# Optimization experiments

Measured on AMD Instinct MI355X. Metric: run time of the kernel, lower is better.

Reference implementation:

```python
import jax, jax.numpy as jnp
import numpy as np
import math

B, S, DIM = 2, 2048, 2048
H, NOPE, ROPE, VDIM = 16, 128, 64, 128
Q_RANK, KV_RANK = 1024, 512
EPS = 1e-6
ROPE_THETA = 10000.0


def setup_inputs() -> dict:
    key = jax.random.key(0)
    ks = jax.random.split(key, 9)
    s = 0.02  # init scale to keep activations/logits well-conditioned
    return {
        "x": jax.random.normal(ks[0], (B, S, DIM), jnp.float32),
        "wq_down": jax.random.normal(ks[1], (Q_RANK, DIM), jnp.float32) * s,
        "q_norm_w": jnp.ones((Q_RANK,), jnp.float32),
        "wq_up": jax.random.normal(ks[2], (H * NOPE, Q_RANK), jnp.float32) * s,
        "wq_rope": jax.random.normal(ks[3], (H * ROPE, Q_RANK), jnp.float32) * s,
        "wkv_down": jax.random.normal(ks[4], (KV_RANK, DIM), jnp.float32) * s,
        "kv_norm_w": jnp.ones((KV_RANK,), jnp.float32),
        "wkv_up": jax.random.normal(ks[5], (H * (NOPE + VDIM), KV_RANK), jnp.float32) * s,
        "wk_rope": jax.random.normal(ks[6], (ROPE, DIM), jnp.float32) * s,
        "wo": jax.random.normal(ks[7], (DIM, H * VDIM), jnp.float32) * s,
    }


def _rmsnorm(x, w, eps=EPS):
    return x * jax.lax.rsqrt(jnp.mean(x * x, axis=-1, keepdims=True) + eps) * w


def _rope_cos_sin(seq_len, head_dim, dtype=jnp.float32):
    inv_freq = 1.0 / (ROPE_THETA ** (jnp.arange(0, head_dim, 2, dtype=jnp.float32) / head_dim))
    t = jnp.arange(seq_len, dtype=jnp.float32)
    freqs = jnp.outer(t, inv_freq)  # [S, head_dim/2]
    return jnp.cos(freqs).astype(dtype), jnp.sin(freqs).astype(dtype)


def _apply_rope(x, cos, sin):
    # x: [B, S, h, d]; cos/sin: [S, d/2]; interleaved (complex) rotation
    x1, x2 = x[..., 0::2], x[..., 1::2]
    c = cos[None, :, None, :]
    s = sin[None, :, None, :]
    o1 = x1 * c - x2 * s
    o2 = x1 * s + x2 * c
    return jnp.stack([o1, o2], axis=-1).reshape(x.shape)


def reference(x, wq_down, q_norm_w, wq_up, wq_rope, wkv_down, kv_norm_w, wkv_up, wk_rope, wo):
    bs, seq_len, _ = x.shape
    # low-rank Q path
    q_c = _rmsnorm(x @ wq_down.T, q_norm_w)                       # [B,S,Qr]
    q_nope = (q_c @ wq_up.T).reshape(bs, seq_len, H, NOPE)
    q_pe = (q_c @ wq_rope.T).reshape(bs, seq_len, H, ROPE)
    # low-rank KV path
    kv_c = _rmsnorm(x @ wkv_down.T, kv_norm_w)                    # [B,S,KVr]
    kv_up = (x_kv := kv_c @ wkv_up.T).reshape(bs, seq_len, H, NOPE + VDIM)
    k_nope, v = kv_up[..., :NOPE], kv_up[..., NOPE:]
    k_rope_shared = (x @ wk_rope.T).reshape(bs, seq_len, 1, ROPE)
    # decoupled RoPE
    cos, sin = _rope_cos_sin(seq_len, ROPE, x.dtype)
    q_pe = _apply_rope(q_pe, cos, sin)
    k_rope_shared = _apply_rope(k_rope_shared, cos, sin)
    k_rope = jnp.broadcast_to(k_rope_shared, (bs, seq_len, H, ROPE))
    q = jnp.concatenate([q_nope, q_pe], axis=-1)                  # [B,S,H,NOPE+ROPE]
    k = jnp.concatenate([k_nope, k_rope], axis=-1)
    scale = 1.0 / math.sqrt(NOPE + ROPE)
    scores = jnp.einsum("bqhd,bkhd->bhqk", q, k) * scale          # [B,H,S,S]
    causal = jnp.tril(jnp.ones((seq_len, seq_len), bool))
    scores = jnp.where(causal[None, None], scores, -jnp.inf)
    probs = jax.nn.softmax(scores.astype(jnp.float32), axis=-1).astype(q.dtype)
    out = jnp.einsum("bhqk,bkhv->bqhv", probs, v).reshape(bs, seq_len, H * VDIM)
    return out @ wo.T
```

## Files before the change

kernel.cpp:

```cpp
#include <hip/hip_runtime.h>
#include <hip/hip_bf16.h>
#include <math.h>

#define B_    2
#define S_    2048
#define DIM_  2048
#define H_    16
#define NOPE_ 128
#define ROPE_ 64
#define VDIM_ 128
#define QR_   1024
#define KVR_  512
#define TOK_  (B_ * S_)

typedef __attribute__((ext_vector_type(8))) short short8;
typedef __attribute__((ext_vector_type(4))) float f32x4;

__device__ __forceinline__ unsigned short f2bf(float f) {
  union { float f; unsigned u; } v; v.f = f;
  unsigned r = v.u + 0x7fffu + ((v.u >> 16) & 1u);
  return (unsigned short)(r >> 16);
}
__device__ __forceinline__ unsigned pk2(float lo, float hi) {
  return (unsigned)f2bf(lo) | ((unsigned)f2bf(hi) << 16);
}

__device__ __forceinline__ void gl_lds16(const unsigned short* g, unsigned short* lds_base) {
  __builtin_amdgcn_global_load_lds(
      (const __attribute__((address_space(1))) void*)g,
      (__attribute__((address_space(3))) void*)lds_base,
      16, 0, 0);
}

__device__ __forceinline__ void store_out(float* p, float v) { *p = v; }
__device__ __forceinline__ void store_out(unsigned short* p, float v) { *p = f2bf(v); }

#define C_X    (TOK_ * DIM_ / 8)
#define C_WQD  (QR_ * DIM_ / 8)
#define C_WKVD (KVR_ * DIM_ / 8)
#define C_WKR  (ROPE_ * DIM_ / 8)
#define C_WQU  (H_ * NOPE_ * QR_ / 8)
#define C_WQR  (H_ * ROPE_ * QR_ / 8)
#define C_WKVU (H_ * (NOPE_ + VDIM_) * KVR_ / 8)
#define C_WO   (DIM_ * H_ * VDIM_ / 8)
#define C_TOT  (C_X + C_WQD + C_WKVD + C_WKR + C_WQU + C_WQR + C_WKVU + C_WO)

__global__ __launch_bounds__(256) void cvt_all(
    const float* __restrict__ x, const float* __restrict__ wqd, const float* __restrict__ wkvd,
    const float* __restrict__ wkr, const float* __restrict__ wqu, const float* __restrict__ wqr,
    const float* __restrict__ wkvu, const float* __restrict__ wo,
    unsigned short* __restrict__ xo, unsigned short* __restrict__ wqdo,
    unsigned short* __restrict__ wkvdo, unsigned short* __restrict__ wkro,
    unsigned short* __restrict__ wquo, unsigned short* __restrict__ wqro,
    unsigned short* __restrict__ wkvuo, unsigned short* __restrict__ woo) {
  int i = blockIdx.x * 256 + threadIdx.x;
  if (i >= C_TOT) return;
  const float* in; unsigned short* out;
  if (i < C_X) { in = x; out = xo; }
  else if ((i -= C_X) < C_WQD) { in = wqd; out = wqdo; }
  else if ((i -= C_WQD) < C_WKVD) { in = wkvd; out = wkvdo; }
  else if ((i -= C_WKVD) < C_WKR) { in = wkr; out = wkro; }
  else if ((i -= C_WKR) < C_WQU) { in = wqu; out = wquo; }
  else if ((i -= C_WQU) < C_WQR) { in = wqr; out = wqro; }
  else if ((i -= C_WQR) < C_WKVU) { in = wkvu; out = wkvuo; }
  else { i -= C_WKVU; in = wo; out = woo; }
  float4 f0 = *(const float4*)(in + (size_t)i * 8);
  float4 f1 = *(const float4*)(in + (size_t)i * 8 + 4);
  uint4 u;
  u.x = pk2(f0.x, f0.y); u.y = pk2(f0.z, f0.w);
  u.z = pk2(f1.x, f1.y); u.w = pk2(f1.z, f1.w);
  *(uint4*)&out[(size_t)i * 8] = u;
}

template <typename OutT, int NT>
__global__ __launch_bounds__(256) void gemm_bf16(const unsigned short* __restrict__ A,
                                                 const unsigned short* __restrict__ Bm,
                                                 OutT* __restrict__ C,
                                                 int M, int N, int K) {
  constexpr int BN = NT * 32;
  __shared__ unsigned short As[128 * 32];
  __shared__ unsigned short Bs[BN * 32];
  const int tid  = threadIdx.x;
  const int wave = tid >> 6;
  const int lane = tid & 63;
  const int quad = lane >> 4;
  const int l15  = lane & 15;
  const int m0 = blockIdx.y * 128;
  const int n0 = blockIdx.x * BN;
  const int wm = (wave & 1) * 64;
  const int wn = (wave >> 1) * (NT * 16);

  f32x4 acc[4][NT];
#pragma unroll
  for (int i = 0; i < 4; ++i)
#pragma unroll
    for (int j = 0; j < NT; ++j) {
      f32x4 z = {0.f, 0.f, 0.f, 0.f};
      acc[i][j] = z;
    }

  for (int k0 = 0; k0 < K; k0 += 32) {
    __syncthreads();
#pragma unroll
    for (int i = 0; i < 2; ++i) {
      const int s = i * 256 + tid;
      const int srow = s >> 2;
      const int sq = (s & 3) ^ ((srow >> 1) & 3);
      gl_lds16(A + (size_t)(m0 + srow) * K + k0 + sq * 8, &As[(i * 256 + wave * 64) * 8]);
    }
#pragma unroll
    for (int i = 0; i < BN / 64; ++i) {
      const int s = i * 256 + tid;
      const int srow = s >> 2;
      const int sq = (s & 3) ^ ((srow >> 1) & 3);
      const int rb = min(n0 + srow, N - 1);
      gl_lds16(Bm + (size_t)rb * K + k0 + sq * 8, &Bs[(i * 256 + wave * 64) * 8]);
    }
    __syncthreads();

    short8 a[4], b[NT];
#pragma unroll
    for (int i = 0; i < 4; ++i) {
      const int r = wm + i * 16 + l15;
      a[i] = *(const short8*)&As[(r * 4 + (quad ^ ((r >> 1) & 3))) * 8];
    }
#pragma unroll
    for (int j = 0; j < NT; ++j) {
      const int r = wn + j * 16 + l15;
      b[j] = *(const short8*)&Bs[(r * 4 + (quad ^ ((r >> 1) & 3))) * 8];
    }
#pragma unroll
    for (int i = 0; i < 4; ++i)
#pragma unroll
      for (int j = 0; j < NT; ++j)
        acc[i][j] = __builtin_amdgcn_mfma_f32_16x16x32_bf16(a[i], b[j], acc[i][j], 0, 0, 0);
  }

#pragma unroll
  for (int i = 0; i < 4; ++i) {
#pragma unroll
    for (int j = 0; j < NT; ++j) {
      const int col = n0 + wn + j * 16 + l15;
      if (col < N) {
#pragma unroll
        for (int r = 0; r < 4; ++r) {
          const int row = m0 + wm + i * 16 + quad * 4 + r;
          store_out(&C[(size_t)row * N + col], acc[i][j][r]);
        }
      }
    }
  }
}

__global__ __launch_bounds__(256) void gemm_down(const unsigned short* __restrict__ A,
                                                 const unsigned short* __restrict__ Bq,
                                                 const unsigned short* __restrict__ Bkv,
                                                 const unsigned short* __restrict__ Bkr,
                                                 float* __restrict__ Cq,
                                                 float* __restrict__ Ckv,
                                                 float* __restrict__ Ckr) {
  constexpr int K = DIM_;
  __shared__ unsigned short As[128 * 32];
  __shared__ unsigned short Bs[128 * 32];
  const int tid  = threadIdx.x;
  const int wave = tid >> 6;
  const int lane = tid & 63;
  const int quad = lane >> 4;
  const int l15  = lane & 15;
  const int m0 = blockIdx.y * 128;
  const int t  = blockIdx.x;

  const unsigned short* Bm; float* C; int n0, NB;
  if (t < 8)       { Bm = Bq;  C = Cq;  n0 = t * 128;        NB = QR_;  }
  else if (t < 12) { Bm = Bkv; C = Ckv; n0 = (t - 8) * 128;  NB = KVR_; }
  else             { Bm = Bkr; C = Ckr; n0 = 0;              NB = ROPE_; }

  const int wm = (wave & 1) * 64;
  const int wn = (wave >> 1) * 64;

  f32x4 acc[4][4];
#pragma unroll
  for (int i = 0; i < 4; ++i)
#pragma unroll
    for (int j = 0; j < 4; ++j) { f32x4 z = {0.f, 0.f, 0.f, 0.f}; acc[i][j] = z; }

  for (int k0 = 0; k0 < K; k0 += 32) {
    __syncthreads();
#pragma unroll
    for (int i = 0; i < 2; ++i) {
      const int s = i * 256 + tid;
      const int srow = s >> 2;
      const int sq = (s & 3) ^ ((srow >> 1) & 3);
      gl_lds16(A + (size_t)(m0 + srow) * K + k0 + sq * 8, &As[(i * 256 + wave * 64) * 8]);
    }
#pragma unroll
    for (int i = 0; i < 2; ++i) {
      const int s = i * 256 + tid;
      const int srow = s >> 2;
      const int sq = (s & 3) ^ ((srow >> 1) & 3);
      const int rb = min(n0 + srow, NB - 1);
      gl_lds16(Bm + (size_t)rb * K + k0 + sq * 8, &Bs[(i * 256 + wave * 64) * 8]);
    }
    __syncthreads();

    short8 a[4], b[4];
#pragma unroll
    for (int i = 0; i < 4; ++i) {
      const int r = wm + i * 16 + l15;
      a[i] = *(const short8*)&As[(r * 4 + (quad ^ ((r >> 1) & 3))) * 8];
    }
#pragma unroll
    for (int j = 0; j < 4; ++j) {
      const int r = wn + j * 16 + l15;
      b[j] = *(const short8*)&Bs[(r * 4 + (quad ^ ((r >> 1) & 3))) * 8];
    }
#pragma unroll
    for (int i = 0; i < 4; ++i)
#pragma unroll
      for (int j = 0; j < 4; ++j)
        acc[i][j] = __builtin_amdgcn_mfma_f32_16x16x32_bf16(a[i], b[j], acc[i][j], 0, 0, 0);
  }

#pragma unroll
  for (int i = 0; i < 4; ++i) {
#pragma unroll
    for (int j = 0; j < 4; ++j) {
      const int col = n0 + wn + j * 16 + l15;
      if (col < NB) {
#pragma unroll
        for (int r = 0; r < 4; ++r) {
          const int row = m0 + wm + i * 16 + quad * 4 + r;
          C[(size_t)row * NB + col] = acc[i][j][r];
        }
      }
    }
  }
}

__global__ __launch_bounds__(256) void gemm_upq(const unsigned short* __restrict__ A,
                                                const unsigned short* __restrict__ Bn,
                                                const unsigned short* __restrict__ Br,
                                                unsigned short* __restrict__ Cn,
                                                float* __restrict__ Cr) {
  constexpr int K = QR_;
  __shared__ unsigned short As[128 * 32];
  __shared__ unsigned short Bs[128 * 32];
  const int tid  = threadIdx.x;
  const int wave = tid >> 6;
  const int lane = tid & 63;
  const int quad = lane >> 4;
  const int l15  = lane & 15;
  const int m0 = blockIdx.y * 128;
  const int t  = blockIdx.x;
  const bool isn = (t < 16);
  const unsigned short* Bm = isn ? Bn : Br;
  const int n0 = isn ? t * 128 : (t - 16) * 128;
  const int NB = isn ? (H_ * NOPE_) : (H_ * ROPE_);

  const int wm = (wave & 1) * 64;
  const int wn = (wave >> 1) * 64;

  f32x4 acc[4][4];
#pragma unroll
  for (int i = 0; i < 4; ++i)
#pragma unroll
    for (int j = 0; j < 4; ++j) { f32x4 z = {0.f, 0.f, 0.f, 0.f}; acc[i][j] = z; }

  for (int k0 = 0; k0 < K; k0 += 32) {
    __syncthreads();
#pragma unroll
    for (int i = 0; i < 2; ++i) {
      const int s = i * 256 + tid;
      const int srow = s >> 2;
      const int sq = (s & 3) ^ ((srow >> 1) & 3);
      gl_lds16(A + (size_t)(m0 + srow) * K + k0 + sq * 8, &As[(i * 256 + wave * 64) * 8]);
    }
#pragma unroll
    for (int i = 0; i < 2; ++i) {
      const int s = i * 256 + tid;
      const int srow = s >> 2;
      const int sq = (s & 3) ^ ((srow >> 1) & 3);
      const int rb = min(n0 + srow, NB - 1);
      gl_lds16(Bm + (size_t)rb * K + k0 + sq * 8, &Bs[(i * 256 + wave * 64) * 8]);
    }
    __syncthreads();

    short8 a[4], b[4];
#pragma unroll
    for (int i = 0; i < 4; ++i) {
      const int r = wm + i * 16 + l15;
      a[i] = *(const short8*)&As[(r * 4 + (quad ^ ((r >> 1) & 3))) * 8];
    }
#pragma unroll
    for (int j = 0; j < 4; ++j) {
      const int r = wn + j * 16 + l15;
      b[j] = *(const short8*)&Bs[(r * 4 + (quad ^ ((r >> 1) & 3))) * 8];
    }
#pragma unroll
    for (int i = 0; i < 4; ++i)
#pragma unroll
      for (int j = 0; j < 4; ++j)
        acc[i][j] = __builtin_amdgcn_mfma_f32_16x16x32_bf16(a[i], b[j], acc[i][j], 0, 0, 0);
  }

#pragma unroll
  for (int i = 0; i < 4; ++i) {
#pragma unroll
    for (int j = 0; j < 4; ++j) {
      const int col = n0 + wn + j * 16 + l15;
#pragma unroll
      for (int r = 0; r < 4; ++r) {
        const int row = m0 + wm + i * 16 + quad * 4 + r;
        if (isn) Cn[(size_t)row * (H_ * NOPE_) + col] = f2bf(acc[i][j][r]);
        else     Cr[(size_t)row * (H_ * ROPE_) + col] = acc[i][j][r];
      }
    }
  }
}

__global__ __launch_bounds__(256) void rmsnorm2(const float* __restrict__ xq,
                                                const float* __restrict__ wq,
                                                unsigned short* __restrict__ oq,
                                                const float* __restrict__ xkv,
                                                const float* __restrict__ wkv,
                                                unsigned short* __restrict__ okv) {
  __shared__ float red[256];
  const bool isq = (blockIdx.y == 0);
  const int n = isq ? QR_ : KVR_;
  const float* x = isq ? xq : xkv;
  const float* w = isq ? wq : wkv;
  unsigned short* o = isq ? oq : okv;
  const int row = blockIdx.x;
  const float* p = x + (size_t)row * n;
  float s = 0.f;
  for (int i = threadIdx.x; i < n; i += 256) { float v = p[i]; s += v * v; }
  red[threadIdx.x] = s;
  __syncthreads();
  for (int off = 128; off > 0; off >>= 1) {
    if (threadIdx.x < off) red[threadIdx.x] += red[threadIdx.x + off];
    __syncthreads();
  }
  const float inv = rsqrtf(red[0] / (float)n + 1e-6f);
  unsigned short* po = o + (size_t)row * n;
  for (int i = threadIdx.x; i < n; i += 256) po[i] = f2bf(p[i] * inv * w[i]);
}

#define PAIRS_Q (TOK_ * H_ * 32)
#define PAIRS_K (TOK_ * 32)

__global__ void rope_all(const float* __restrict__ qin, unsigned short* __restrict__ qout,
                         const float* __restrict__ kin, unsigned short* __restrict__ kout) {
  int idx = blockIdx.x * blockDim.x + threadIdx.x;
  if (idx >= PAIRS_Q + PAIRS_K) return;
  int heads, id;
  const float* xin; unsigned short* xout;
  if (idx < PAIRS_Q) { heads = H_; xin = qin; xout = qout; id = idx; }
  else { heads = 1; xin = kin; xout = kout; id = idx - PAIRS_Q; }
  const int i = id & 31;
  const int h = (id >> 5) % heads;
  const int row = id / (32 * heads);
  const int pos = row & (S_ - 1);
  const float freq = expf(-9.210340371976184f * (float)i / 32.0f);
  const float ang = (float)pos * freq;
  const float c = cosf(ang), sn = sinf(ang);
  const float* p = xin + ((size_t)row * heads + h) * 64 + 2 * i;
  unsigned short* q = xout + ((size_t)row * heads + h) * 64 + 2 * i;
  const float x1 = p[0], x2 = p[1];
  q[0] = f2bf(x1 * c - x2 * sn);
  q[1] = f2bf(x1 * sn + x2 * c);
}

__global__ __launch_bounds__(256) void transpose_v(const unsigned short* __restrict__ kv_up,
                                                   unsigned short* __restrict__ vt_g) {
  __shared__ unsigned short T[128 * 72];
  const int tid = threadIdx.x;
  const int k0 = blockIdx.x * 64;
  const int h = blockIdx.y, b = blockIdx.z;
  const size_t tok0 = (size_t)b * S_;
#pragma unroll
  for (int i = 0; i < 2; ++i) {
    const int u = i * 256 + tid;
    const int kp = u >> 4, c8 = u & 15;
    const unsigned short* p0 =
        kv_up + (tok0 + k0 + 2 * kp) * (size_t)(H_ * 256) + h * 256 + NOPE_ + c8 * 8;
    union { uint4 v; unsigned short s[8]; } r0, r1;
    r0.v = *(const uint4*)p0;
    r1.v = *(const uint4*)(p0 + H_ * 256);
#pragma unroll
    for (int j = 0; j < 8; ++j)
      *(unsigned*)&T[(c8 * 8 + j) * 72 + 2 * kp] = (unsigned)r0.s[j] | ((unsigned)r1.s[j] << 16);
  }
  __syncthreads();
#pragma unroll
  for (int i = 0; i < 4; ++i) {
    const int sl = i * 256 + tid;
    const int f = sl >> 3, c = sl & 7;
    *(uint4*)(vt_g + ((size_t)(b * H_ + h) * 128 + f) * S_ + k0 + c * 8) =
        *(const uint4*)&T[f * 72 + c * 8];
  }
}

#define LV 72

__global__ __launch_bounds__(512) void flash_attn_mfma(const unsigned short* q_nope,
                                                       const unsigned short* __restrict__ q_pe,
                                                       const unsigned short* __restrict__ kv_up,
                                                       const unsigned short* __restrict__ k_rope,
                                                       const unsigned short* __restrict__ vt_g,
                                                       unsigned short* attn_o) {
  __shared__ unsigned short Ksn[2][64 * 16 * 8];
  __shared__ unsigned short Ksr[2][64 * 8 * 8];
  __shared__ unsigned short Vt[128 * 8 * 8];
  __shared__ unsigned short Ps[128 * LV];

  const int tid  = threadIdx.x;
  const int wave = tid >> 6;
  const int lane = tid & 63;
  const int quad = lane >> 4;
  const int l15  = lane & 15;
  const int pair = blockIdx.x;
  const int h  = blockIdx.y;
  const int b  = blockIdx.z;
  const size_t tok0 = (size_t)b * S_;
  const float scale2 = 0.07216878364870323f * 1.4426950408889634f;
  const int qtA = 15 - pair;
  const int qtB = pair;
  const int n0  = 2 * qtA + 2;

  auto LOADQ = [&](short8* qf, int qt) {
    const size_t qrow = tok0 + qt * 128 + wave * 16 + l15;
    const unsigned short* pn = q_nope + qrow * (size_t)(H_ * NOPE_) + h * NOPE_;
    const unsigned short* pp = q_pe + qrow * (size_t)(H_ * ROPE_) + h * ROPE_;
#pragma unroll
    for (int s = 0; s < 4; ++s) qf[s] = *(const short8*)(pn + s * 32 + quad * 8);
#pragma unroll
    for (int s = 4; s < 6; ++s) qf[s] = *(const short8*)(pp + (s - 4) * 32 + quad * 8);
  };

  auto STAGE_K = [&](int bi, int kt) {
    const int k0 = kt * 64;
#pragma unroll
    for (int i = 0; i < 2; ++i) {
      const int sl = i * 512 + tid;
      const int key = sl >> 4;
      const int c = (sl & 15) ^ (key & 15);
      gl_lds16(kv_up + (tok0 + k0 + key) * (size_t)(H_ * 256) + h * 256 + c * 8,
               &Ksn[bi][(i * 512 + wave * 64) * 8]);
    }
    {
      const int sl = tid;
      const int key = sl >> 3;
      const int c = (sl & 7) ^ (key & 7);
      gl_lds16(k_rope + (tok0 + k0 + key) * (size_t)ROPE_ + c * 8,
               &Ksr[bi][(wave * 64) * 8]);
    }
  };
  auto STAGE_V = [&](int kt) {
    const int k0 = kt * 64;
#pragma unroll
    for (int i = 0; i < 2; ++i) {
      const int sl = i * 512 + tid;
      const int f = sl >> 3;
      const int c = (sl & 7) ^ (f & 7);
      gl_lds16(vt_g + ((size_t)(b * H_ + h) * 128 + f) * S_ + k0 + c * 8,
               &Vt[(i * 512 + wave * 64) * 8]);
    }
  };

  short8 qf[6];
  LOADQ(qf, qtA);

  float m_st[4], l_st[4];
  f32x4 o[8];
#pragma unroll
  for (int r = 0; r < 4; ++r) { m_st[r] = -1e30f; l_st[r] = 0.f; }
#pragma unroll
  for (int nt = 0; nt < 8; ++nt) { f32x4 z = {0.f, 0.f, 0.f, 0.f}; o[nt] = z; }

  auto EPI = [&](int qt) {
    float invl[4];
#pragma unroll
    for (int r = 0; r < 4; ++r) invl[r] = 1.f / l_st[r];
#pragma unroll
    for (int nt = 0; nt < 8; ++nt)
#pragma unroll
      for (int r = 0; r < 4; ++r) {
        const size_t row = tok0 + qt * 128 + wave * 16 + quad * 4 + r;
        attn_o[row * (size_t)(H_ * VDIM_) + h * VDIM_ + nt * 16 + l15] =
            f2bf(o[nt][r] * invl[r]);
      }
  };

  STAGE_K(0, 0);

  for (int it = 0; it < 34; ++it) {
    const int cur = it & 1;
    const int nxt = cur ^ 1;
    const bool ph1 = (it >= n0);
    const int qt = ph1 ? qtB : qtA;
    const int kt = ph1 ? (it - n0) : it;
    const bool last = (it + 1 >= 34);
    const bool active = !(kt == 2 * qt + 1 && wave < 4);

    __builtin_amdgcn_s_barrier();
    asm volatile("" ::: "memory");

    STAGE_V(kt);
    if (!last) {
      const bool p1n = (it + 1 >= n0);
      const int kt2 = p1n ? (it + 1 - n0) : (it + 1);
      STAGE_K(nxt, kt2);
      asm volatile("s_waitcnt vmcnt(5)" ::: "memory");
    } else {
      asm volatile("s_waitcnt vmcnt(2)" ::: "memory");
    }
    __builtin_amdgcn_s_barrier();
    asm volatile("" ::: "memory");
    __builtin_amdgcn_sched_barrier(0);

    if (active) {
      f32x4 sacc[4];
#pragma unroll
      for (int nt = 0; nt < 4; ++nt) { f32x4 z = {0.f, 0.f, 0.f, 0.f}; sacc[nt] = z; }
      __builtin_amdgcn_s_setprio(1);
#pragma unroll
      for (int s = 0; s < 4; ++s) {
#pragma unroll
        for (int nt = 0; nt < 4; ++nt) {
          const int key = nt * 16 + l15;
          short8 kb = *(const short8*)&Ksn[cur][(key * 16 + ((s * 4 + quad) ^ (key & 15))) * 8];
          sacc[nt] = __builtin_amdgcn_mfma_f32_16x16x32_bf16(qf[s], kb, sacc[nt], 0, 0, 0);
        }
      }
#pragma unroll
      for (int s = 4; s < 6; ++s) {
#pragma unroll
        for (int nt = 0; nt < 4; ++nt) {
          const int key = nt * 16 + l15;
          short8 kb = *(const short8*)&Ksr[cur][(key * 8 + (((s - 4) * 4 + quad) ^ (key & 7))) * 8];
          sacc[nt] = __builtin_amdgcn_mfma_f32_16x16x32_bf16(qf[s], kb, sacc[nt], 0, 0, 0);
        }
      }
      __builtin_amdgcn_s_setprio(0);

      float sc[4][4];
#pragma unroll
      for (int nt = 0; nt < 4; ++nt)
#pragma unroll
        for (int r = 0; r < 4; ++r) sc[nt][r] = sacc[nt][r] * scale2;
      if (kt >= 2 * qt) {
        const int koff = (kt - 2 * qt) * 64;
        const int rw = wave * 16 + quad * 4;
#pragma unroll
        for (int nt = 0; nt < 4; ++nt)
#pragma unroll
          for (int r = 0; r < 4; ++r)
            if ((koff + nt * 16 + l15) > (rw + r)) sc[nt][r] = -1e30f;
      }

      float mt[4];
#pragma unroll
      for (int r = 0; r < 4; ++r)
        mt[r] = fmaxf(fmaxf(sc[0][r], sc[1][r]), fmaxf(sc[2][r], sc[3][r]));
#pragma unroll
      for (int mask = 1; mask <= 8; mask <<= 1)
#pragma unroll
        for (int r = 0; r < 4; ++r) mt[r] = fmaxf(mt[r], __shfl_xor(mt[r], mask, 64));

      float al[4], rs[4];
#pragma unroll
      for (int r = 0; r < 4; ++r) {
        const float mn = fmaxf(m_st[r], mt[r]);
        al[r] = exp2f(m_st[r] - mn);
        m_st[r] = mn;
        rs[r] = 0.f;
      }
#pragma unroll
      for (int nt = 0; nt < 4; ++nt)
#pragma unroll
        for (int r = 0; r < 4; ++r) {
          const float p = exp2f(sc[nt][r] - m_st[r]);
          sc[nt][r] = p;
          rs[r] += p;
        }
#pragma unroll
      for (int mask = 1; mask <= 8; mask <<= 1)
#pragma unroll
        for (int r = 0; r < 4; ++r) rs[r] += __shfl_xor(rs[r], mask, 64);
#pragma unroll
      for (int r = 0; r < 4; ++r) l_st[r] = l_st[r] * al[r] + rs[r];

#pragma unroll
      for (int nt = 0; nt < 4; ++nt)
#pragma unroll
        for (int r = 0; r < 4; ++r)
          Ps[(wave * 16 + quad * 4 + r) * LV + nt * 16 + l15] = f2bf(sc[nt][r]);
      __builtin_amdgcn_wave_barrier();

#pragma unroll
      for (int nt = 0; nt < 8; ++nt)
#pragma unroll
        for (int r = 0; r < 4; ++r) o[nt][r] *= al[r];
    }

    if (!last) {
      asm volatile("s_waitcnt vmcnt(3)" ::: "memory");
    } else {
      asm volatile("s_waitcnt vmcnt(0)" ::: "memory");
    }
    __builtin_amdgcn_s_barrier();
    asm volatile("" ::: "memory");
    __builtin_amdgcn_sched_barrier(0);

    if (active) {
      __builtin_amdgcn_s_setprio(1);
#pragma unroll
      for (int s = 0; s < 2; ++s) {
        short8 pa = *(const short8*)&Ps[(wave * 16 + l15) * LV + s * 32 + quad * 8];
#pragma unroll
        for (int nt = 0; nt < 8; ++nt) {
          const int f = nt * 16 + l15;
          short8 vb = *(const short8*)&Vt[(f * 8 + ((s * 4 + quad) ^ (f & 7))) * 8];
          o[nt] = __builtin_amdgcn_mfma_f32_16x16x32_bf16(pa, vb, o[nt], 0, 0, 0);
        }
      }
      __builtin_amdgcn_s_setprio(0);
    }

    if (it == n0 - 1) {
      EPI(qtA);
      LOADQ(qf, qtB);
#pragma unroll
      for (int r = 0; r < 4; ++r) { m_st[r] = -1e30f; l_st[r] = 0.f; }
#pragma unroll
      for (int nt = 0; nt < 8; ++nt) { f32x4 z = {0.f, 0.f, 0.f, 0.f}; o[nt] = z; }
    }
  }

  EPI(qtB);
}

extern "C" void kernel_launch(void* const* d_in, const int* in_sizes, int n_in,
                              void* d_out, int out_size, void* d_ws, size_t ws_size,
                              hipStream_t stream) {
  (void)in_sizes; (void)n_in;
  const float* x         = (const float*)d_in[0];
  const float* wq_down   = (const float*)d_in[1];
  const float* q_norm_w  = (const float*)d_in[2];
  const float* wq_up     = (const float*)d_in[3];
  const float* wq_rope   = (const float*)d_in[4];
  const float* wkv_down  = (const float*)d_in[5];
  const float* kv_norm_w = (const float*)d_in[6];
  const float* wkv_up    = (const float*)d_in[7];
  const float* wk_rope   = (const float*)d_in[8];
  const float* wo        = (const float*)d_in[9];
  float* out = (float*)d_out;

  const size_t SZ_XBF   = (size_t)TOK_ * DIM_ * 2;
  const size_t SZ_WQD   = (size_t)QR_ * DIM_ * 2;
  const size_t SZ_WKVD  = (size_t)KVR_ * DIM_ * 2;
  const size_t SZ_WKR   = (size_t)ROPE_ * DIM_ * 2;
  const size_t SZ_WQU   = (size_t)H_ * NOPE_ * QR_ * 2;
  const size_t SZ_WQR   = (size_t)H_ * ROPE_ * QR_ * 2;
  const size_t SZ_WKVU  = (size_t)H_ * (NOPE_ + VDIM_) * KVR_ * 2;
  const size_t SZ_WO    = (size_t)DIM_ * H_ * VDIM_ * 2;
  const size_t SZ_QC    = (size_t)TOK_ * QR_ * 4;
  const size_t SZ_KVC   = (size_t)TOK_ * KVR_ * 4;
  const size_t SZ_QCN   = (size_t)TOK_ * QR_ * 2;
  const size_t SZ_KVCN  = (size_t)TOK_ * KVR_ * 2;
  const size_t SZ_QNOPE = (size_t)TOK_ * H_ * NOPE_ * 2;
  const size_t SZ_QPEB  = (size_t)TOK_ * H_ * ROPE_ * 2;
  const size_t SZ_KRF   = (size_t)TOK_ * ROPE_ * 4;
  const size_t SZ_KRB   = (size_t)TOK_ * ROPE_ * 2;
  const size_t SZ_KVUP  = (size_t)TOK_ * H_ * (NOPE_ + VDIM_) * 2;
  const size_t NEED = SZ_XBF + SZ_WQD + SZ_WKVD + SZ_WKR + SZ_WQU + SZ_WQR + SZ_WKVU +
                      SZ_WO + SZ_QC + SZ_KVC + SZ_QCN + SZ_KVCN + SZ_QNOPE + SZ_QPEB +
                      SZ_KRF + SZ_KRB + SZ_KVUP;
  if (ws_size < NEED) {
    hipMemsetAsync(d_out, 0, (size_t)out_size * sizeof(float), stream);
    return;
  }
  char* p = (char*)d_ws;
  unsigned short* x_bf    = (unsigned short*)p; p += SZ_XBF;
  unsigned short* wqd_bf  = (unsigned short*)p; p += SZ_WQD;
  unsigned short* wkvd_bf = (unsigned short*)p; p += SZ_WKVD;
  unsigned short* wkr_bf  = (unsigned short*)p; p += SZ_WKR;
  unsigned short* wqu_bf  = (unsigned short*)p; p += SZ_WQU;
  unsigned short* wqr_bf  = (unsigned short*)p; p += SZ_WQR;
  unsigned short* wkvu_bf = (unsigned short*)p; p += SZ_WKVU;
  unsigned short* wo_bf   = (unsigned short*)p; p += SZ_WO;
  float*          q_c     = (float*)p;          p += SZ_QC;
  float*          kv_c    = (float*)p;          p += SZ_KVC;
  unsigned short* q_cn    = (unsigned short*)p; p += SZ_QCN;
  unsigned short* kv_cn   = (unsigned short*)p; p += SZ_KVCN;
  unsigned short* q_nope  = (unsigned short*)p; p += SZ_QNOPE;
  unsigned short* q_pe_bf = (unsigned short*)p; p += SZ_QPEB;
  float*          k_ropef = (float*)p;          p += SZ_KRF;
  unsigned short* k_ropeb = (unsigned short*)p; p += SZ_KRB;
  unsigned short* kv_upbf = (unsigned short*)p; p += SZ_KVUP;
  float*          q_pe_f  = q_c;
  unsigned short* vt_g    = (unsigned short*)q_c;
  unsigned short* attn_o  = q_nope;

  const dim3 blk(256);

  cvt_all<<<(C_TOT + 255) / 256, blk, 0, stream>>>(
      x, wq_down, wkv_down, wk_rope, wq_up, wq_rope, wkv_up, wo,
      x_bf, wqd_bf, wkvd_bf, wkr_bf, wqu_bf, wqr_bf, wkvu_bf, wo_bf);

  gemm_down<<<dim3(13, TOK_ / 128), blk, 0, stream>>>(x_bf, wqd_bf, wkvd_bf, wkr_bf,
                                                      q_c, kv_c, k_ropef);

  rmsnorm2<<<dim3(TOK_, 2), blk, 0, stream>>>(q_c, q_norm_w, q_cn, kv_c, kv_norm_w, kv_cn);

  gemm_upq<<<dim3(24, TOK_ / 128), blk, 0, stream>>>(q_cn, wqu_bf, wqr_bf, q_nope, q_pe_f);

  gemm_bf16<unsigned short, 4><<<dim3(H_ * (NOPE_ + VDIM_) / 128, TOK_ / 128), blk, 0, stream>>>(
      kv_cn, wkvu_bf, kv_upbf, TOK_, H_ * (NOPE_ + VDIM_), KVR_);

  rope_all<<<(PAIRS_Q + PAIRS_K + 255) / 256, blk, 0, stream>>>(q_pe_f, q_pe_bf, k_ropef, k_ropeb);

  transpose_v<<<dim3(S_ / 64, H_, B_), blk, 0, stream>>>(kv_upbf, vt_g);

  flash_attn_mfma<<<dim3(8, H_, B_), dim3(512), 0, stream>>>(q_nope, q_pe_bf, kv_upbf, k_ropeb, vt_g, attn_o);

  gemm_bf16<float, 4><<<dim3(DIM_ / 128, TOK_ / 128), blk, 0, stream>>>(attn_o, wo_bf, out, TOK_, DIM_, H_ * VDIM_);
}
```

Baseline: 475.9 us.

## Use 128-key tiles in flash attention and remap blocks to heads

Doubles the key/value tile per iteration from 64 to 128 keys, halving the loop count and the barriers and waitcnt synchronisations per block. The causal-boundary wave-skip logic is removed because a 128-key tile now aligns with the 128-row query tile. P is written to LDS in two halves to reuse the existing Ps buffer. Block indices are also remapped so that consecutive blocks spread across heads and batches, which changes L2 locality and scheduling. The cost is roughly double the LDS footprint per block and more registers for the 8 score accumulators, which may lower occupancy.

```diff
diff --git a/kernel.cpp b/kernel.cpp
--- a/kernel.cpp
+++ b/kernel.cpp
@@ -408,9 +408,9 @@
                                                        const unsigned short* __restrict__ k_rope,
                                                        const unsigned short* __restrict__ vt_g,
                                                        unsigned short* attn_o) {
-  __shared__ unsigned short Ksn[2][64 * 16 * 8];
-  __shared__ unsigned short Ksr[2][64 * 8 * 8];
-  __shared__ unsigned short Vt[128 * 8 * 8];
+  __shared__ unsigned short Ksn[2][128 * 16 * 8];
+  __shared__ unsigned short Ksr[2][128 * 8 * 8];
+  __shared__ unsigned short Vt[128 * 16 * 8];
   __shared__ unsigned short Ps[128 * LV];
 
   const int tid  = threadIdx.x;
@@ -418,14 +418,18 @@
   const int lane = tid & 63;
   const int quad = lane >> 4;
   const int l15  = lane & 15;
-  const int pair = blockIdx.x;
-  const int h  = blockIdx.y;
-  const int b  = blockIdx.z;
+  const int l   = blockIdx.x + 8 * blockIdx.y + 128 * blockIdx.z;
+  const int c_  = l & 7;
+  const int m_  = l >> 3;
+  const int pair = m_ & 7;
+  const int hb   = c_ * 4 + (m_ >> 3);
+  const int h  = hb & 15;
+  const int b  = hb >> 4;
   const size_t tok0 = (size_t)b * S_;
   const float scale2 = 0.07216878364870323f * 1.4426950408889634f;
   const int qtA = 15 - pair;
   const int qtB = pair;
-  const int n0  = 2 * qtA + 2;
+  const int nA  = qtA + 1;
 
   auto LOADQ = [&](short8* qf, int qt) {
     const size_t qrow = tok0 + qt * 128 + wave * 16 + l15;
@@ -438,30 +442,31 @@
   };
 
   auto STAGE_K = [&](int bi, int kt) {
-    const int k0 = kt * 64;
-#pragma unroll
-    for (int i = 0; i < 2; ++i) {
+    const int k0 = kt * 128;
+#pragma unroll
+    for (int i = 0; i < 4; ++i) {
       const int sl = i * 512 + tid;
       const int key = sl >> 4;
       const int c = (sl & 15) ^ (key & 15);
       gl_lds16(kv_up + (tok0 + k0 + key) * (size_t)(H_ * 256) + h * 256 + c * 8,
                &Ksn[bi][(i * 512 + wave * 64) * 8]);
     }
-    {
-      const int sl = tid;
+#pragma unroll
+    for (int i = 0; i < 2; ++i) {
+      const int sl = i * 512 + tid;
       const int key = sl >> 3;
       const int c = (sl & 7) ^ (key & 7);
       gl_lds16(k_rope + (tok0 + k0 + key) * (size_t)ROPE_ + c * 8,
-               &Ksr[bi][(wave * 64) * 8]);
+               &Ksr[bi][(i * 512 + wave * 64) * 8]);
     }
   };
   auto STAGE_V = [&](int kt) {
-    const int k0 = kt * 64;
-#pragma unroll
-    for (int i = 0; i < 2; ++i) {
+    const int k0 = kt * 128;
+#pragma unroll
+    for (int i = 0; i < 4; ++i) {
       const int sl = i * 512 + tid;
-      const int f = sl >> 3;
-      const int c = (sl & 7) ^ (f & 7);
+      const int f = sl >> 4;
+      const int c = (sl & 15) ^ (f & 15);
       gl_lds16(vt_g + ((size_t)(b * H_ + h) * 128 + f) * S_ + k0 + c * 8,
                &Vt[(i * 512 + wave * 64) * 8]);
     }
@@ -493,118 +498,117 @@
 
   STAGE_K(0, 0);
 
-  for (int it = 0; it < 34; ++it) {
+  for (int it = 0; it < 17; ++it) {
     const int cur = it & 1;
     const int nxt = cur ^ 1;
-    const bool ph1 = (it >= n0);
+    const bool ph1 = (it >= nA);
     const int qt = ph1 ? qtB : qtA;
-    const int kt = ph1 ? (it - n0) : it;
-    const bool last = (it + 1 >= 34);
-    const bool active = !(kt == 2 * qt + 1 && wave < 4);
+    const int kt = ph1 ? (it - nA) : it;
+    const bool last = (it + 1 >= 17);
 
     __builtin_amdgcn_s_barrier();
     asm volatile("" ::: "memory");
 
     STAGE_V(kt);
     if (!last) {
-      const bool p1n = (it + 1 >= n0);
-      const int kt2 = p1n ? (it + 1 - n0) : (it + 1);
+      const int it2 = it + 1;
+      const int kt2 = (it2 >= nA) ? (it2 - nA) : it2;
       STAGE_K(nxt, kt2);
-      asm volatile("s_waitcnt vmcnt(5)" ::: "memory");
+      asm volatile("s_waitcnt vmcnt(10)" ::: "memory");
     } else {
-      asm volatile("s_waitcnt vmcnt(2)" ::: "memory");
+      asm volatile("s_waitcnt vmcnt(4)" ::: "memory");
     }
     __builtin_amdgcn_s_barrier();
     asm volatile("" ::: "memory");
     __builtin_amdgcn_sched_barrier(0);
 
-    if (active) {
-      f32x4 sacc[4];
-#pragma unroll
-      for (int nt = 0; nt < 4; ++nt) { f32x4 z = {0.f, 0.f, 0.f, 0.f}; sacc[nt] = z; }
-      __builtin_amdgcn_s_setprio(1);
-#pragma unroll
-      for (int s = 0; s < 4; ++s) {
-#pragma unroll
-        for (int nt = 0; nt < 4; ++nt) {
-          const int key = nt * 16 + l15;
-          short8 kb = *(const short8*)&Ksn[cur][(key * 16 + ((s * 4 + quad) ^ (key & 15))) * 8];
-          sacc[nt] = __builtin_amdgcn_mfma_f32_16x16x32_bf16(qf[s], kb, sacc[nt], 0, 0, 0);
-        }
-      }
-#pragma unroll
-      for (int s = 4; s < 6; ++s) {
-#pragma unroll
-        for (int nt = 0; nt < 4; ++nt) {
-          const int key = nt * 16 + l15;
-          short8 kb = *(const short8*)&Ksr[cur][(key * 8 + (((s - 4) * 4 + quad) ^ (key & 7))) * 8];
-          sacc[nt] = __builtin_amdgcn_mfma_f32_16x16x32_bf16(qf[s], kb, sacc[nt], 0, 0, 0);
-        }
-      }
-      __builtin_amdgcn_s_setprio(0);
-
-      float sc[4][4];
-#pragma unroll
-      for (int nt = 0; nt < 4; ++nt)
-#pragma unroll
-        for (int r = 0; r < 4; ++r) sc[nt][r] = sacc[nt][r] * scale2;
-      if (kt >= 2 * qt) {
-        const int koff = (kt - 2 * qt) * 64;
-        const int rw = wave * 16 + quad * 4;
-#pragma unroll
-        for (int nt = 0; nt < 4; ++nt)
-#pragma unroll
-          for (int r = 0; r < 4; ++r)
-            if ((koff + nt * 16 + l15) > (rw + r)) sc[nt][r] = -1e30f;
-      }
-
-      float mt[4];
+    f32x4 sacc[8];
+#pragma unroll
+    for (int nt = 0; nt < 8; ++nt) { f32x4 z = {0.f, 0.f, 0.f, 0.f}; sacc[nt] = z; }
+    __builtin_amdgcn_s_setprio(1);
+#pragma unroll
+    for (int s = 0; s < 4; ++s) {
+#pragma unroll
+      for (int nt = 0; nt < 8; ++nt) {
+        const int key = nt * 16 + l15;
+        short8 kb = *(const short8*)&Ksn[cur][(key * 16 + ((s * 4 + quad) ^ (key & 15))) * 8];
+        sacc[nt] = __builtin_amdgcn_mfma_f32_16x16x32_bf16(qf[s], kb, sacc[nt], 0, 0, 0);
+      }
+    }
+#pragma unroll
+    for (int s = 4; s < 6; ++s) {
+#pragma unroll
+      for (int nt = 0; nt < 8; ++nt) {
+        const int key = nt * 16 + l15;
+        short8 kb = *(const short8*)&Ksr[cur][(key * 8 + (((s - 4) * 4 + quad) ^ (key & 7))) * 8];
+        sacc[nt] = __builtin_amdgcn_mfma_f32_16x16x32_bf16(qf[s], kb, sacc[nt], 0, 0, 0);
+      }
+    }
+    __builtin_amdgcn_s_setprio(0);
+
+    float sc[8][4];
+#pragma unroll
+    for (int nt = 0; nt < 8; ++nt)
+#pragma unroll
+      for (int r = 0; r < 4; ++r) sc[nt][r] = sacc[nt][r] * scale2;
+    if (kt == qt) {
+      const int rw = wave * 16 + quad * 4;
+#pragma unroll
+      for (int nt = 0; nt < 8; ++nt)
+#pragma unroll
+        for (int r = 0; r < 4; ++r)
+          if ((nt * 16 + l15) > (rw + r)) sc[nt][r] = -1e30f;
+    }
+
+    float mt[4];
+#pragma unroll
+    for (int r = 0; r < 4; ++r) {
+      float a0 = fmaxf(fmaxf(sc[0][r], sc[1][r]), fmaxf(sc[2][r], sc[3][r]));
+      float a1 = fmaxf(fmaxf(sc[4][r], sc[5][r]), fmaxf(sc[6][r], sc[7][r]));
+      mt[r] = fmaxf(a0, a1);
+    }
+#pragma unroll
+    for (int mask = 1; mask <= 8; mask <<= 1)
+#pragma unroll
+      for (int r = 0; r < 4; ++r) mt[r] = fmaxf(mt[r], __shfl_xor(mt[r], mask, 64));
+
+    float al[4], rs[4];
+#pragma unroll
+    for (int r = 0; r < 4; ++r) {
+      const float mn = fmaxf(m_st[r], mt[r]);
+      al[r] = exp2f(m_st[r] - mn);
+      m_st[r] = mn;
+      rs[r] = 0.f;
+    }
+#pragma unroll
+    for (int nt = 0; nt < 8; ++nt)
+#pragma unroll
+      for (int r = 0; r < 4; ++r) {
+        const float p = exp2f(sc[nt][r] - m_st[r]);
+        sc[nt][r] = p;
+        rs[r] += p;
+      }
+#pragma unroll
+    for (int mask = 1; mask <= 8; mask <<= 1)
+#pragma unroll
+      for (int r = 0; r < 4; ++r) rs[r] += __shfl_xor(rs[r], mask, 64);
+#pragma unroll
+    for (int r = 0; r < 4; ++r) l_st[r] = l_st[r] * al[r] + rs[r];
+
+#pragma unroll
+    for (int nt = 0; nt < 4; ++nt)
 #pragma unroll
       for (int r = 0; r < 4; ++r)
-        mt[r] = fmaxf(fmaxf(sc[0][r], sc[1][r]), fmaxf(sc[2][r], sc[3][r]));
-#pragma unroll
-      for (int mask = 1; mask <= 8; mask <<= 1)
-#pragma unroll
-        for (int r = 0; r < 4; ++r) mt[r] = fmaxf(mt[r], __shfl_xor(mt[r], mask, 64));
-
-      float al[4], rs[4];
-#pragma unroll
-      for (int r = 0; r < 4; ++r) {
-        const float mn = fmaxf(m_st[r], mt[r]);
-        al[r] = exp2f(m_st[r] - mn);
-        m_st[r] = mn;
-        rs[r] = 0.f;
-      }
-#pragma unroll
-      for (int nt = 0; nt < 4; ++nt)
-#pragma unroll
-        for (int r = 0; r < 4; ++r) {
-          const float p = exp2f(sc[nt][r] - m_st[r]);
-          sc[nt][r] = p;
-          rs[r] += p;
-        }
-#pragma unroll
-      for (int mask = 1; mask <= 8; mask <<= 1)
-#pragma unroll
-        for (int r = 0; r < 4; ++r) rs[r] += __shfl_xor(rs[r], mask, 64);
-#pragma unroll
-      for (int r = 0; r < 4; ++r) l_st[r] = l_st[r] * al[r] + rs[r];
-
-#pragma unroll
-      for (int nt = 0; nt < 4; ++nt)
-#pragma unroll
-        for (int r = 0; r < 4; ++r)
-          Ps[(wave * 16 + quad * 4 + r) * LV + nt * 16 + l15] = f2bf(sc[nt][r]);
-      __builtin_amdgcn_wave_barrier();
-
-#pragma unroll
-      for (int nt = 0; nt < 8; ++nt)
-#pragma unroll
-        for (int r = 0; r < 4; ++r) o[nt][r] *= al[r];
-    }
+        Ps[(wave * 16 + quad * 4 + r) * LV + nt * 16 + l15] = f2bf(sc[nt][r]);
+    __builtin_amdgcn_wave_barrier();
+
+#pragma unroll
+    for (int nt = 0; nt < 8; ++nt)
+#pragma unroll
+      for (int r = 0; r < 4; ++r) o[nt][r] *= al[r];
 
     if (!last) {
-      asm volatile("s_waitcnt vmcnt(3)" ::: "memory");
+      asm volatile("s_waitcnt vmcnt(6)" ::: "memory");
     } else {
       asm volatile("s_waitcnt vmcnt(0)" ::: "memory");
     }
@@ -612,22 +616,40 @@
     asm volatile("" ::: "memory");
     __builtin_amdgcn_sched_barrier(0);
 
-    if (active) {
-      __builtin_amdgcn_s_setprio(1);
-#pragma unroll
-      for (int s = 0; s < 2; ++s) {
-        short8 pa = *(const short8*)&Ps[(wave * 16 + l15) * LV + s * 32 + quad * 8];
-#pragma unroll
-        for (int nt = 0; nt < 8; ++nt) {
-          const int f = nt * 16 + l15;
-          short8 vb = *(const short8*)&Vt[(f * 8 + ((s * 4 + quad) ^ (f & 7))) * 8];
-          o[nt] = __builtin_amdgcn_mfma_f32_16x16x32_bf16(pa, vb, o[nt], 0, 0, 0);
-        }
-      }
-      __builtin_amdgcn_s_setprio(0);
-    }
-
-    if (it == n0 - 1) {
+    __builtin_amdgcn_s_setprio(1);
+#pragma unroll
+    for (int kb = 0; kb < 2; ++kb) {
+      short8 pa = *(const short8*)&Ps[(wave * 16 + l15) * LV + kb * 32 + quad * 8];
+#pragma unroll
+      for (int nt = 0; nt < 8; ++nt) {
+        const int f = nt * 16 + l15;
+        short8 vb = *(const short8*)&Vt[(f * 16 + ((kb * 4 + quad) ^ (f & 15))) * 8];
+        o[nt] = __builtin_amdgcn_mfma_f32_16x16x32_bf16(pa, vb, o[nt], 0, 0, 0);
+      }
+    }
+    __builtin_amdgcn_s_setprio(0);
+
+#pragma unroll
+    for (int nt = 4; nt < 8; ++nt)
+#pragma unroll
+      for (int r = 0; r < 4; ++r)
+        Ps[(wave * 16 + quad * 4 + r) * LV + (nt - 4) * 16 + l15] = f2bf(sc[nt][r]);
+    __builtin_amdgcn_wave_barrier();
+
+    __builtin_amdgcn_s_setprio(1);
+#pragma unroll
+    for (int kb = 2; kb < 4; ++kb) {
+      short8 pa = *(const short8*)&Ps[(wave * 16 + l15) * LV + (kb - 2) * 32 + quad * 8];
+#pragma unroll
+      for (int nt = 0; nt < 8; ++nt) {
+        const int f = nt * 16 + l15;
+        short8 vb = *(const short8*)&Vt[(f * 16 + ((kb * 4 + quad) ^ (f & 15))) * 8];
+        o[nt] = __builtin_amdgcn_mfma_f32_16x16x32_bf16(pa, vb, o[nt], 0, 0, 0);
+      }
+    }
+    __builtin_amdgcn_s_setprio(0);
+
+    if (it == nA - 1) {
       EPI(qtA);
       LOADQ(qf, qtB);
 #pragma unroll
```

Result: faster. 439.6 us (-7.6%).
